# Optimization experiments

Measured on AMD Instinct MI355X. Metric: run time of the kernel, lower is better.

Reference implementation:

```python
import jax, jax.numpy as jnp
import numpy as np

D_MODEL = 1024
NUM_HEADS = 16
D_K = D_MODEL // NUM_HEADS
NEG = -10000.0


def setup_inputs() -> dict:
    key = jax.random.key(0)
    ks = jax.random.split(key, 8)
    B, S = 2, 2048
    query = jax.random.normal(ks[0], (B, S, D_MODEL), dtype=jnp.float32)
    key_t = jax.random.normal(ks[1], (B, S, D_MODEL), dtype=jnp.float32)
    value = jax.random.normal(ks[2], (B, S, D_MODEL), dtype=jnp.float32)
    mask = jax.random.randint(ks[3], (B, S), 0, 2, dtype=jnp.int32)
    scale = 1.0 / np.sqrt(D_MODEL)
    Wq = jax.random.normal(ks[4], (D_MODEL, D_MODEL), dtype=jnp.float32) * scale
    Wk = jax.random.normal(ks[5], (D_MODEL, D_MODEL), dtype=jnp.float32) * scale
    Wv = jax.random.normal(ks[6], (D_MODEL, D_MODEL), dtype=jnp.float32) * scale
    Wo = jax.random.normal(ks[7], (D_MODEL, D_MODEL), dtype=jnp.float32) * scale
    return {"query": query, "key": key_t, "value": value, "mask": mask,
            "Wq": Wq, "Wk": Wk, "Wv": Wv, "Wo": Wo}


def reference(query, key, value, mask, Wq, Wk, Wv, Wo):
    B, Sq, _ = query.shape
    Sk = key.shape[1]
    # Linear projections (torch Linear: x @ W.T), split heads -> [B,H,S,d_k]
    def proj(x, W, S):
        return (x @ W.T).reshape(B, S, NUM_HEADS, D_K).transpose(0, 2, 1, 3)
    Q = proj(query, Wq, Sq)
    K = proj(key, Wk, Sk)
    V = proj(value, Wv, Sk)
    # scores [B,H,Sq,Sk]
    scores = jnp.einsum("bhqd,bhkd->bhqk", Q, K) / jnp.sqrt(jnp.float32(D_K))
    # padding mask [B,Sk] -> [B,1,1,Sk]
    pad = mask[:, None, None, :]
    scores = jnp.where(pad == 0, NEG, scores)
    # causal mask (mask_future=True)
    causal = jnp.tril(jnp.ones((Sq, Sk), dtype=bool))
    scores = jnp.where(causal, scores, NEG)
    probs = jax.nn.softmax(scores, axis=-1)  # dropout p=0.0 -> identity
    out = jnp.einsum("bhqk,bhkd->bhqd", probs, V)
    out = out.transpose(0, 2, 1, 3).reshape(B, Sq, D_MODEL)
    return out @ Wo.T
```

## Files before the change

kernel.cpp:

```cpp
#include <hip/hip_runtime.h>
#include <hip/hip_bf16.h>
#include <math.h>

typedef __attribute__((ext_vector_type(8))) short s16x8;
typedef __attribute__((ext_vector_type(4))) float f32x4;

#define MFMA16(a,b,c) __builtin_amdgcn_mfma_f32_16x16x32_bf16((a),(b),(c),0,0,0)

#define GLD16(gp, lp) __builtin_amdgcn_global_load_lds( \
  (const __attribute__((address_space(1))) unsigned int*)(gp), \
  (__attribute__((address_space(3))) unsigned int*)(lp), 16, 0, 0)

static __device__ __forceinline__ unsigned short f2bu(float f) {
  __hip_bfloat16 h = __float2bfloat16(f);
  unsigned short u; __builtin_memcpy(&u, &h, 2); return u;
}
static __device__ __forceinline__ float b2f(unsigned short u) {
  unsigned int x = ((unsigned int)u) << 16; float f; __builtin_memcpy(&f, &x, 4); return f;
}
static __device__ __forceinline__ unsigned int cvtpk(float lo, float hi) {
  unsigned int r;
  asm("v_cvt_pk_bf16_f32 %0, %1, %2" : "=v"(r) : "v"(lo), "v"(hi));
  return r;
}

__global__ __launch_bounds__(256) void cast_all(const float* __restrict__ q, const float* __restrict__ k,
                                                const float* __restrict__ v,
                                                const float* __restrict__ Wq, const float* __restrict__ Wk,
                                                const float* __restrict__ Wv, const float* __restrict__ Wo,
                                                const int* __restrict__ mask,
                                                unsigned short* __restrict__ qc, unsigned short* __restrict__ kc,
                                                unsigned short* __restrict__ vc,
                                                unsigned short* __restrict__ wq, unsigned short* __restrict__ wk,
                                                unsigned short* __restrict__ wv, unsigned short* __restrict__ wo,
                                                int* __restrict__ fu, unsigned int* __restrict__ pm) {
  const float SCALE2 = 0.125f * 1.4426950408889634f;
  const int y = blockIdx.y;
  if (y == 7) {
    if (blockIdx.x >= 2) return;
    const int S = 2048;
    int b = blockIdx.x;
    __shared__ int red[256];
    int best = S;
    for (int kk = threadIdx.x; kk < 1024; kk += 256) {
      int m0 = mask[b * S + 2 * kk], m1 = mask[b * S + 2 * kk + 1];
      pm[b * 1024 + kk] = (m0 ? 0xFFFFu : 0u) | (m1 ? 0xFFFF0000u : 0u);
      if (m1) best = min(best, 2 * kk + 1);
      if (m0) best = min(best, 2 * kk);
    }
    red[threadIdx.x] = best;
    __syncthreads();
    for (int s = 128; s > 0; s >>= 1) {
      if (threadIdx.x < s) red[threadIdx.x] = min(red[threadIdx.x], red[threadIdx.x + s]);
      __syncthreads();
    }
    if (threadIdx.x == 0) fu[b] = red[0];
    return;
  }
  const float* in; unsigned short* out; int n4; float scl = 1.0f;
  switch (y) {
    case 0: in = q;  out = qc; n4 = 1048576; break;
    case 1: in = k;  out = kc; n4 = 1048576; break;
    case 2: in = v;  out = vc; n4 = 1048576; break;
    case 3: in = Wq; out = wq; n4 = 262144; scl = SCALE2; break;
    case 4: in = Wk; out = wk; n4 = 262144; break;
    case 5: in = Wv; out = wv; n4 = 262144; break;
    default: in = Wo; out = wo; n4 = 262144; break;
  }
  int i = blockIdx.x * 256 + threadIdx.x;
  if (i < n4) {
    float4 val = *(const float4*)(in + (size_t)i * 4);
    uint2 pk;
    pk.x = cvtpk(val.x * scl, val.y * scl);
    pk.y = cvtpk(val.z * scl, val.w * scl);
    *(uint2*)(out + (size_t)i * 4) = pk;
  }
}

static __device__ __forceinline__ void gemm_core(const unsigned short* __restrict__ Aw,
                                                 const unsigned short* __restrict__ Bw,
                                                 int m0, int n0,
                                                 f32x4 (&acc)[4][4],
                                                 unsigned short (*As)[64], unsigned short (*Bs)[64]) {
  const int K = 1024;
  const int tid = threadIdx.x;
  const int lane = tid & 63, wave = tid >> 6;
  const int wm = wave >> 1, wn = wave & 1;
  const int row16 = lane & 15, kgrp = lane >> 4;
  const int srow = lane >> 3, sslot = (lane & 7) ^ srow;
  const int sw = row16 & 7;

  for (int k0 = 0; k0 < K; k0 += 64) {
#pragma unroll
    for (int i = 0; i < 4; i++) {
      int rr = (wave * 4 + i) * 8 + srow;
      GLD16(Aw + (size_t)(m0 + rr) * K + k0 + sslot * 8, (char*)As + (wave * 4 + i) * 1024);
      GLD16(Bw + (size_t)(n0 + rr) * K + k0 + sslot * 8, (char*)Bs + (wave * 4 + i) * 1024);
    }
    __syncthreads();

#pragma unroll
    for (int kk = 0; kk < 2; kk++) {
      s16x8 af[4], bfr[4];
#pragma unroll
      for (int mi = 0; mi < 4; mi++) {
        int rr = wm * 64 + mi * 16 + row16;
        af[mi] = *(const s16x8*)((char*)&As[rr][0] + ((kk * 4 + kgrp) ^ sw) * 16);
      }
#pragma unroll
      for (int ni = 0; ni < 4; ni++) {
        int rr = wn * 64 + ni * 16 + row16;
        bfr[ni] = *(const s16x8*)((char*)&Bs[rr][0] + ((kk * 4 + kgrp) ^ sw) * 16);
      }
#pragma unroll
      for (int mi = 0; mi < 4; mi++)
#pragma unroll
        for (int ni = 0; ni < 4; ni++)
          acc[mi][ni] = MFMA16(af[mi], bfr[ni], acc[mi][ni]);
    }
    __syncthreads();
  }
}

__global__ __launch_bounds__(256) void qkv_gemm(const unsigned short* __restrict__ qc,
                                                const unsigned short* __restrict__ kc,
                                                const unsigned short* __restrict__ vc,
                                                const unsigned short* __restrict__ Wqb,
                                                const unsigned short* __restrict__ Wkb,
                                                const unsigned short* __restrict__ Wvb,
                                                unsigned short* __restrict__ Qb,
                                                unsigned short* __restrict__ Kb,
                                                unsigned short* __restrict__ Vt) {
  __shared__ unsigned short As[128][64];
  __shared__ unsigned short Bs[128][64];
  const int xcd = blockIdx.x & 7, u = blockIdx.x >> 3;
  const int g = xcd * 12 + (u >> 3);
  const int z = g >> 5, mstrip = g & 31;
  const int m0 = mstrip * 128, n0 = (u & 7) * 128;

  const unsigned short* A = (z == 0) ? qc : (z == 1) ? kc : vc;
  const unsigned short* Bw = (z == 0) ? Wqb : (z == 1) ? Wkb : Wvb;

  f32x4 acc[4][4] = {};
  gemm_core(A, Bw, m0, n0, acc, As, Bs);

  const int lane = threadIdx.x & 63, wave = threadIdx.x >> 6;
  const int wm = wave >> 1, wn = wave & 1;
  const int row16 = lane & 15, kgrp = lane >> 4;

  if (z < 2) {
    unsigned short* C = z ? Kb : Qb;
#pragma unroll
    for (int mi = 0; mi < 4; mi++)
#pragma unroll
      for (int ni = 0; ni < 4; ni++)
#pragma unroll
        for (int r = 0; r < 4; r++) {
          int row = m0 + wm * 64 + mi * 16 + kgrp * 4 + r;
          int col = n0 + wn * 64 + ni * 16 + row16;
          C[(size_t)row * 1024 + col] = f2bu(acc[mi][ni][r]);
        }
  } else {
#pragma unroll
    for (int mi = 0; mi < 4; mi++)
#pragma unroll
      for (int ni = 0; ni < 4; ni++) {
        int mb = m0 + wm * 64 + mi * 16 + kgrp * 4;
        int col = n0 + wn * 64 + ni * 16 + row16;
        int bb = mb >> 11, s = mb & 2047;
        uint2 pk;
        pk.x = cvtpk(acc[mi][ni][0], acc[mi][ni][1]);
        pk.y = cvtpk(acc[mi][ni][2], acc[mi][ni][3]);
        *(uint2*)&Vt[(((size_t)(bb * 1024 + col)) << 11) + s] = pk;
      }
  }
}

__global__ __launch_bounds__(256) void gemm_wo(const unsigned short* __restrict__ A,
                                               const unsigned short* __restrict__ Bw,
                                               float* __restrict__ C) {
  __shared__ unsigned short As[128][64];
  __shared__ unsigned short Bs[128][64];
  const int xcd = blockIdx.x & 7, u = blockIdx.x >> 3;
  const int g = xcd * 4 + (u >> 3);
  const int m0 = g * 128, n0 = (u & 7) * 128;

  f32x4 acc[4][4] = {};
  gemm_core(A, Bw, m0, n0, acc, As, Bs);

  const int lane = threadIdx.x & 63, wave = threadIdx.x >> 6;
  const int wm = wave >> 1, wn = wave & 1;
  const int row16 = lane & 15, kgrp = lane >> 4;
#pragma unroll
  for (int mi = 0; mi < 4; mi++)
#pragma unroll
    for (int ni = 0; ni < 4; ni++)
#pragma unroll
      for (int r = 0; r < 4; r++) {
        int row = m0 + wm * 64 + mi * 16 + kgrp * 4 + r;
        int col = n0 + wn * 64 + ni * 16 + row16;
        C[(size_t)row * 1024 + col] = acc[mi][ni][r];
      }
}

__global__ __launch_bounds__(256) void reduce_vt(const unsigned short* __restrict__ Vt,
                                                 float* __restrict__ vsum) {
  __shared__ float red[256];
  const unsigned short* p = Vt + ((size_t)blockIdx.x << 11) + threadIdx.x * 8;
  uint4 u = *(const uint4*)p;
  float s = b2f((unsigned short)(u.x & 0xffff));
  s += b2f((unsigned short)(u.x >> 16));
  s += b2f((unsigned short)(u.y & 0xffff));
  s += b2f((unsigned short)(u.y >> 16));
  s += b2f((unsigned short)(u.z & 0xffff));
  s += b2f((unsigned short)(u.z >> 16));
  s += b2f((unsigned short)(u.w & 0xffff));
  s += b2f((unsigned short)(u.w >> 16));
  red[threadIdx.x] = s;
  __syncthreads();
  for (int st = 128; st > 0; st >>= 1) {
    if (threadIdx.x < st) red[threadIdx.x] += red[threadIdx.x + st];
    __syncthreads();
  }
  if (threadIdx.x == 0) vsum[blockIdx.x] = red[0];
}

__global__ __launch_bounds__(256) void flash_attn8(const unsigned short* __restrict__ Q,
                                                   const unsigned short* __restrict__ Kp,
                                                   const unsigned short* __restrict__ Vt,
                                                   const unsigned int* __restrict__ pm,
                                                   const int* __restrict__ fu,
                                                   const float* __restrict__ vsum,
                                                   unsigned short* __restrict__ O) {
  const int S = 2048, DM = 1024;
  const int bid = blockIdx.x;
  const int qt = 31 - (bid >> 5);
  const int bh = bid & 31;
  const int b = bh >> 4, h = bh & 15;
  const int tid = threadIdx.x, lane = tid & 63, wave = tid >> 6;
  const int row16 = lane & 15, kgrp = lane >> 4;

  __shared__ unsigned short Ks[2][64][64];
  __shared__ unsigned short Vs[2][64][64];
  __shared__ unsigned short Ps[4][16][64];

  const size_t base = ((size_t)b * S) * DM + h * 64;
  const size_t vtb = ((size_t)(b * 1024 + h * 64)) * S;
  const unsigned int* pmb = pm + b * 1024;

  const int srow = lane >> 3;
  const int sslot = (lane & 7) ^ srow;
  const int sw = row16 & 7;

  const int q0 = qt * 64 + wave * 16;
  const int qg = q0 + row16;
  const int nt = qt + 1;

  s16x8 qf0 = *(const s16x8*)&Q[base + (size_t)qg * DM + kgrp * 8];
  s16x8 qf1 = *(const s16x8*)&Q[base + (size_t)qg * DM + 32 + kgrp * 8];

  const short ONE = 0x3F80;
  const s16x8 ones8 = {ONE, ONE, ONE, ONE, ONE, ONE, ONE, ONE};

  f32x4 oacc[4] = {};
  f32x4 lacc = {};
  float m_run = -1e30f;

  auto stage = [&](int t, int bf) {
    const int kb = t * 64;
#pragma unroll
    for (int c2 = 0; c2 < 2; c2++) {
      const int r = wave * 16 + c2 * 8 + srow;
      GLD16(Kp + base + (size_t)(kb + r) * DM + sslot * 8,
            (char*)&Ks[bf][0][0] + (wave * 2 + c2) * 1024);
      GLD16(Vt + vtb + (size_t)r * S + kb + sslot * 8,
            (char*)&Vs[bf][0][0] + (wave * 2 + c2) * 1024);
    }
  };

  stage(0, 0);
  asm volatile("s_waitcnt vmcnt(0)" ::: "memory");
  __syncthreads();

  int cur = 0;
  for (int t = 0; t < nt; ++t) {
    if (t + 1 < nt) stage(t + 1, cur ^ 1);
    const int kb = t * 64;

    uint2 pmv[4];
#pragma unroll
    for (int nf = 0; nf < 4; nf++)
      pmv[nf] = *(const uint2*)&pmb[(kb + nf * 16 + kgrp * 4) >> 1];

    f32x4 sc[4];
    __builtin_amdgcn_s_setprio(1);
#pragma unroll
    for (int nf = 0; nf < 4; nf++) {
      const int rr = nf * 16 + row16;
      s16x8 k0 = *(const s16x8*)&Ks[cur][rr][(kgrp ^ sw) * 8];
      s16x8 k1 = *(const s16x8*)&Ks[cur][rr][((4 + kgrp) ^ sw) * 8];
      f32x4 a = {};
      a = MFMA16(k0, qf0, a);
      a = MFMA16(k1, qf1, a);
      sc[nf] = a;
    }
    __builtin_amdgcn_s_setprio(0);

    if (t == nt - 1) {
#pragma unroll
      for (int nf = 0; nf < 4; nf++) {
        const int kbase = kb + nf * 16 + kgrp * 4;
#pragma unroll
        for (int r = 0; r < 4; r++)
          if (kbase + r > qg) sc[nf][r] = -30000.0f;
      }
    }

    float a0 = fmaxf(fmaxf(sc[0][0], sc[0][1]), sc[0][2]);
    float a1 = fmaxf(fmaxf(sc[0][3], sc[1][0]), sc[1][1]);
    float a2 = fmaxf(fmaxf(sc[1][2], sc[1][3]), sc[2][0]);
    float a3 = fmaxf(fmaxf(sc[2][1], sc[2][2]), sc[2][3]);
    float a4 = fmaxf(fmaxf(sc[3][0], sc[3][1]), sc[3][2]);
    float b0 = fmaxf(fmaxf(a0, a1), a2);
    float b1 = fmaxf(fmaxf(a3, a4), sc[3][3]);
    float tmax = fmaxf(b0, b1);

    if (__any(tmax > m_run)) {
      float wmax = fmaxf(tmax, __shfl_xor(tmax, 16));
      wmax = fmaxf(wmax, __shfl_xor(wmax, 32));
      float alpha = __builtin_exp2f(m_run - wmax);
      m_run = wmax;
      lacc[0] *= alpha; lacc[1] *= alpha; lacc[2] *= alpha; lacc[3] *= alpha;
#pragma unroll
      for (int nf2 = 0; nf2 < 4; nf2++)
#pragma unroll
        for (int r = 0; r < 4; r++) oacc[nf2][r] *= alpha;
    }

#pragma unroll
    for (int nf = 0; nf < 4; nf++)
#pragma unroll
      for (int r = 0; r < 4; r++)
        sc[nf][r] = __builtin_exp2f(sc[nf][r] - m_run);

#pragma unroll
    for (int nf = 0; nf < 4; nf++) {
      uint2 pk;
      pk.x = cvtpk(sc[nf][0], sc[nf][1]) & pmv[nf].x;
      pk.y = cvtpk(sc[nf][2], sc[nf][3]) & pmv[nf].y;
      const int slot = (nf * 2 + (kgrp >> 1)) ^ sw;
      *(uint2*)((char*)&Ps[wave][row16][0] + slot * 16 + (kgrp & 1) * 8) = pk;
    }
    s16x8 pf0 = *(const s16x8*)((char*)&Ps[wave][row16][0] + (kgrp ^ sw) * 16);
    s16x8 pf1 = *(const s16x8*)((char*)&Ps[wave][row16][0] + ((4 + kgrp) ^ sw) * 16);

    __builtin_amdgcn_s_setprio(1);
    lacc = MFMA16(ones8, pf0, lacc);
    lacc = MFMA16(ones8, pf1, lacc);
#pragma unroll
    for (int nf2 = 0; nf2 < 4; nf2++) {
      const int rr = nf2 * 16 + row16;
      s16x8 v0 = *(const s16x8*)&Vs[cur][rr][(kgrp ^ sw) * 8];
      s16x8 v1 = *(const s16x8*)&Vs[cur][rr][((4 + kgrp) ^ sw) * 8];
      oacc[nf2] = MFMA16(v0, pf0, oacc[nf2]);
      oacc[nf2] = MFMA16(v1, pf1, oacc[nf2]);
    }
    __builtin_amdgcn_s_setprio(0);

    asm volatile("s_waitcnt vmcnt(0)" ::: "memory");
    __syncthreads();
    cur ^= 1;
  }

  const int fub = fu[b];
  const float* vs = vsum + b * DM + h * 64;
  const float rl = 1.0f / lacc[0];
#pragma unroll
  for (int nf2 = 0; nf2 < 4; nf2++) {
    const int d0 = nf2 * 16 + kgrp * 4;
    float v0 = oacc[nf2][0] * rl, v1 = oacc[nf2][1] * rl;
    float v2 = oacc[nf2][2] * rl, v3 = oacc[nf2][3] * rl;
    if (qg < fub) {
      float4 vv = *(const float4*)&vs[d0];
      v0 = vv.x * (1.0f / 2048.0f);
      v1 = vv.y * (1.0f / 2048.0f);
      v2 = vv.z * (1.0f / 2048.0f);
      v3 = vv.w * (1.0f / 2048.0f);
    }
    uint2 pk;
    pk.x = cvtpk(v0, v1);
    pk.y = cvtpk(v2, v3);
    *(uint2*)&O[base + (size_t)qg * DM + d0] = pk;
  }
}

extern "C" void kernel_launch(void* const* d_in, const int* in_sizes, int n_in,
                              void* d_out, int out_size, void* d_ws, size_t ws_size,
                              hipStream_t stream) {
  const float* q    = (const float*)d_in[0];
  const float* k    = (const float*)d_in[1];
  const float* v    = (const float*)d_in[2];
  const int*   mask = (const int*)d_in[3];
  const float* Wq   = (const float*)d_in[4];
  const float* Wk   = (const float*)d_in[5];
  const float* Wv   = (const float*)d_in[6];
  const float* Wo   = (const float*)d_in[7];
  float* out = (float*)d_out;
  char* ws = (char*)d_ws;

  unsigned short* Wqb  = (unsigned short*)(ws + (size_t)0);
  unsigned short* Wkb  = (unsigned short*)(ws + ((size_t)2 << 20));
  unsigned short* Wvb  = (unsigned short*)(ws + ((size_t)4 << 20));
  unsigned short* Wob  = (unsigned short*)(ws + ((size_t)6 << 20));
  unsigned short* vc   = (unsigned short*)(ws + ((size_t)8 << 20));
  unsigned short* attn = (unsigned short*)(ws + ((size_t)8 << 20));
  unsigned short* Qb   = (unsigned short*)(ws + ((size_t)16 << 20));
  unsigned short* Kb   = (unsigned short*)(ws + ((size_t)24 << 20));
  unsigned short* Vt   = (unsigned short*)(ws + ((size_t)32 << 20));
  float* vsum          = (float*)(ws + ((size_t)40 << 20));
  int*   fub           = (int*)(ws + ((size_t)40 << 20) + (64 << 10));
  unsigned int* pm32   = (unsigned int*)(ws + ((size_t)40 << 20) + (68 << 10));
  unsigned short* qc   = (unsigned short*)d_out;
  unsigned short* kc   = (unsigned short*)d_out + 4194304;

  cast_all<<<dim3(4096, 8), 256, 0, stream>>>(q, k, v, Wq, Wk, Wv, Wo, mask,
                                              qc, kc, vc, Wqb, Wkb, Wvb, Wob, fub, pm32);

  qkv_gemm<<<768, 256, 0, stream>>>(qc, kc, vc, Wqb, Wkb, Wvb, Qb, Kb, Vt);

  reduce_vt<<<2048, 256, 0, stream>>>(Vt, vsum);

  flash_attn8<<<1024, 256, 0, stream>>>(Qb, Kb, Vt, pm32, fub, vsum, attn);

  gemm_wo<<<256, 256, 0, stream>>>(attn, Wob, out);
}
```

Baseline: 140.9 us.

## Process two 16-row query fragments per wave to double K/V tile reuse

Each wave now handles 32 query rows (two 16-row MFMA fragments) instead of 16, so each block covers a 128-row query tile and the grid halves to 512 blocks. Every K and V tile staged into LDS, and every K/V fragment read from LDS, now feeds twice as many MFMAs, which cuts global and LDS traffic per unit of compute. The causal mask now applies to the last two key tiles. The cost is higher register pressure from doubled accumulators and query fragments, fewer blocks to spread across CUs, and coarser causal load imbalance.

```diff
diff --git a/kernel.cpp b/kernel.cpp
--- a/kernel.cpp
+++ b/kernel.cpp
@@ -225,7 +225,7 @@
   if (threadIdx.x == 0) vsum[blockIdx.x] = red[0];
 }
 
-__global__ __launch_bounds__(256) void flash_attn8(const unsigned short* __restrict__ Q,
+__global__ __launch_bounds__(256) void flash_attn9(const unsigned short* __restrict__ Q,
                                                    const unsigned short* __restrict__ Kp,
                                                    const unsigned short* __restrict__ Vt,
                                                    const unsigned int* __restrict__ pm,
@@ -234,7 +234,7 @@
                                                    unsigned short* __restrict__ O) {
   const int S = 2048, DM = 1024;
   const int bid = blockIdx.x;
-  const int qt = 31 - (bid >> 5);
+  const int qtile = 15 - (bid >> 5);
   const int bh = bid & 31;
   const int b = bh >> 4, h = bh & 15;
   const int tid = threadIdx.x, lane = tid & 63, wave = tid >> 6;
@@ -242,7 +242,7 @@
 
   __shared__ unsigned short Ks[2][64][64];
   __shared__ unsigned short Vs[2][64][64];
-  __shared__ unsigned short Ps[4][16][64];
+  __shared__ unsigned short Ps[4][32][64];
 
   const size_t base = ((size_t)b * S) * DM + h * 64;
   const size_t vtb = ((size_t)(b * 1024 + h * 64)) * S;
@@ -252,19 +252,23 @@
   const int sslot = (lane & 7) ^ srow;
   const int sw = row16 & 7;
 
-  const int q0 = qt * 64 + wave * 16;
-  const int qg = q0 + row16;
-  const int nt = qt + 1;
-
-  s16x8 qf0 = *(const s16x8*)&Q[base + (size_t)qg * DM + kgrp * 8];
-  s16x8 qf1 = *(const s16x8*)&Q[base + (size_t)qg * DM + 32 + kgrp * 8];
+  const int q0w = qtile * 128 + wave * 32;
+  int qgF[2]; qgF[0] = q0w + row16; qgF[1] = q0w + 16 + row16;
+  const int nt = qtile * 2 + 2;
+
+  s16x8 qf[2][2];
+#pragma unroll
+  for (int f = 0; f < 2; f++) {
+    qf[f][0] = *(const s16x8*)&Q[base + (size_t)qgF[f] * DM + kgrp * 8];
+    qf[f][1] = *(const s16x8*)&Q[base + (size_t)qgF[f] * DM + 32 + kgrp * 8];
+  }
 
   const short ONE = 0x3F80;
   const s16x8 ones8 = {ONE, ONE, ONE, ONE, ONE, ONE, ONE, ONE};
 
-  f32x4 oacc[4] = {};
-  f32x4 lacc = {};
-  float m_run = -1e30f;
+  f32x4 oacc[2][4] = {};
+  f32x4 lacc[2] = {};
+  float m_run[2] = {-1e30f, -1e30f};
 
   auto stage = [&](int t, int bf) {
     const int kb = t * 64;
@@ -292,78 +296,92 @@
     for (int nf = 0; nf < 4; nf++)
       pmv[nf] = *(const uint2*)&pmb[(kb + nf * 16 + kgrp * 4) >> 1];
 
-    f32x4 sc[4];
+    f32x4 sc[2][4];
     __builtin_amdgcn_s_setprio(1);
 #pragma unroll
     for (int nf = 0; nf < 4; nf++) {
       const int rr = nf * 16 + row16;
       s16x8 k0 = *(const s16x8*)&Ks[cur][rr][(kgrp ^ sw) * 8];
       s16x8 k1 = *(const s16x8*)&Ks[cur][rr][((4 + kgrp) ^ sw) * 8];
-      f32x4 a = {};
-      a = MFMA16(k0, qf0, a);
-      a = MFMA16(k1, qf1, a);
-      sc[nf] = a;
+      f32x4 aA = {}, aB = {};
+      aA = MFMA16(k0, qf[0][0], aA);
+      aA = MFMA16(k1, qf[0][1], aA);
+      aB = MFMA16(k0, qf[1][0], aB);
+      aB = MFMA16(k1, qf[1][1], aB);
+      sc[0][nf] = aA; sc[1][nf] = aB;
     }
     __builtin_amdgcn_s_setprio(0);
 
-    if (t == nt - 1) {
+    if (t >= nt - 2) {
+#pragma unroll
+      for (int f = 0; f < 2; f++)
+#pragma unroll
+        for (int nf = 0; nf < 4; nf++) {
+          const int kbase = kb + nf * 16 + kgrp * 4;
+#pragma unroll
+          for (int r = 0; r < 4; r++)
+            if (kbase + r > qgF[f]) sc[f][nf][r] = -30000.0f;
+        }
+    }
+
+    s16x8 pf[2][2];
+#pragma unroll
+    for (int f = 0; f < 2; f++) {
+      float a0 = fmaxf(fmaxf(sc[f][0][0], sc[f][0][1]), sc[f][0][2]);
+      float a1 = fmaxf(fmaxf(sc[f][0][3], sc[f][1][0]), sc[f][1][1]);
+      float a2 = fmaxf(fmaxf(sc[f][1][2], sc[f][1][3]), sc[f][2][0]);
+      float a3 = fmaxf(fmaxf(sc[f][2][1], sc[f][2][2]), sc[f][2][3]);
+      float a4 = fmaxf(fmaxf(sc[f][3][0], sc[f][3][1]), sc[f][3][2]);
+      float b0 = fmaxf(fmaxf(a0, a1), a2);
+      float b1 = fmaxf(fmaxf(a3, a4), sc[f][3][3]);
+      float tmax = fmaxf(b0, b1);
+
+      if (__any(tmax > m_run[f])) {
+        float wmax = fmaxf(tmax, __shfl_xor(tmax, 16));
+        wmax = fmaxf(wmax, __shfl_xor(wmax, 32));
+        float alpha = __builtin_exp2f(m_run[f] - wmax);
+        m_run[f] = wmax;
+        lacc[f][0] *= alpha; lacc[f][1] *= alpha; lacc[f][2] *= alpha; lacc[f][3] *= alpha;
+#pragma unroll
+        for (int nf2 = 0; nf2 < 4; nf2++)
+#pragma unroll
+          for (int r = 0; r < 4; r++) oacc[f][nf2][r] *= alpha;
+      }
+
+#pragma unroll
+      for (int nf = 0; nf < 4; nf++)
+#pragma unroll
+        for (int r = 0; r < 4; r++)
+          sc[f][nf][r] = __builtin_exp2f(sc[f][nf][r] - m_run[f]);
+
+      char* prow = (char*)&Ps[wave][f * 16 + row16][0];
 #pragma unroll
       for (int nf = 0; nf < 4; nf++) {
-        const int kbase = kb + nf * 16 + kgrp * 4;
-#pragma unroll
-        for (int r = 0; r < 4; r++)
-          if (kbase + r > qg) sc[nf][r] = -30000.0f;
-      }
-    }
-
-    float a0 = fmaxf(fmaxf(sc[0][0], sc[0][1]), sc[0][2]);
-    float a1 = fmaxf(fmaxf(sc[0][3], sc[1][0]), sc[1][1]);
-    float a2 = fmaxf(fmaxf(sc[1][2], sc[1][3]), sc[2][0]);
-    float a3 = fmaxf(fmaxf(sc[2][1], sc[2][2]), sc[2][3]);
-    float a4 = fmaxf(fmaxf(sc[3][0], sc[3][1]), sc[3][2]);
-    float b0 = fmaxf(fmaxf(a0, a1), a2);
-    float b1 = fmaxf(fmaxf(a3, a4), sc[3][3]);
-    float tmax = fmaxf(b0, b1);
-
-    if (__any(tmax > m_run)) {
-      float wmax = fmaxf(tmax, __shfl_xor(tmax, 16));
-      wmax = fmaxf(wmax, __shfl_xor(wmax, 32));
-      float alpha = __builtin_exp2f(m_run - wmax);
-      m_run = wmax;
-      lacc[0] *= alpha; lacc[1] *= alpha; lacc[2] *= alpha; lacc[3] *= alpha;
-#pragma unroll
-      for (int nf2 = 0; nf2 < 4; nf2++)
-#pragma unroll
-        for (int r = 0; r < 4; r++) oacc[nf2][r] *= alpha;
-    }
-
-#pragma unroll
-    for (int nf = 0; nf < 4; nf++)
-#pragma unroll
-      for (int r = 0; r < 4; r++)
-        sc[nf][r] = __builtin_exp2f(sc[nf][r] - m_run);
-
-#pragma unroll
-    for (int nf = 0; nf < 4; nf++) {
-      uint2 pk;
-      pk.x = cvtpk(sc[nf][0], sc[nf][1]) & pmv[nf].x;
-      pk.y = cvtpk(sc[nf][2], sc[nf][3]) & pmv[nf].y;
-      const int slot = (nf * 2 + (kgrp >> 1)) ^ sw;
-      *(uint2*)((char*)&Ps[wave][row16][0] + slot * 16 + (kgrp & 1) * 8) = pk;
-    }
-    s16x8 pf0 = *(const s16x8*)((char*)&Ps[wave][row16][0] + (kgrp ^ sw) * 16);
-    s16x8 pf1 = *(const s16x8*)((char*)&Ps[wave][row16][0] + ((4 + kgrp) ^ sw) * 16);
+        uint2 pk;
+        pk.x = cvtpk(sc[f][nf][0], sc[f][nf][1]) & pmv[nf].x;
+        pk.y = cvtpk(sc[f][nf][2], sc[f][nf][3]) & pmv[nf].y;
+        const int slot = (nf * 2 + (kgrp >> 1)) ^ sw;
+        *(uint2*)(prow + slot * 16 + (kgrp & 1) * 8) = pk;
+      }
+      pf[f][0] = *(const s16x8*)(prow + (kgrp ^ sw) * 16);
+      pf[f][1] = *(const s16x8*)(prow + ((4 + kgrp) ^ sw) * 16);
+    }
 
     __builtin_amdgcn_s_setprio(1);
-    lacc = MFMA16(ones8, pf0, lacc);
-    lacc = MFMA16(ones8, pf1, lacc);
+#pragma unroll
+    for (int f = 0; f < 2; f++) {
+      lacc[f] = MFMA16(ones8, pf[f][0], lacc[f]);
+      lacc[f] = MFMA16(ones8, pf[f][1], lacc[f]);
+    }
 #pragma unroll
     for (int nf2 = 0; nf2 < 4; nf2++) {
       const int rr = nf2 * 16 + row16;
       s16x8 v0 = *(const s16x8*)&Vs[cur][rr][(kgrp ^ sw) * 8];
       s16x8 v1 = *(const s16x8*)&Vs[cur][rr][((4 + kgrp) ^ sw) * 8];
-      oacc[nf2] = MFMA16(v0, pf0, oacc[nf2]);
-      oacc[nf2] = MFMA16(v1, pf1, oacc[nf2]);
+      oacc[0][nf2] = MFMA16(v0, pf[0][0], oacc[0][nf2]);
+      oacc[0][nf2] = MFMA16(v1, pf[0][1], oacc[0][nf2]);
+      oacc[1][nf2] = MFMA16(v0, pf[1][0], oacc[1][nf2]);
+      oacc[1][nf2] = MFMA16(v1, pf[1][1], oacc[1][nf2]);
     }
     __builtin_amdgcn_s_setprio(0);
 
@@ -374,23 +392,27 @@
 
   const int fub = fu[b];
   const float* vs = vsum + b * DM + h * 64;
-  const float rl = 1.0f / lacc[0];
-#pragma unroll
-  for (int nf2 = 0; nf2 < 4; nf2++) {
-    const int d0 = nf2 * 16 + kgrp * 4;
-    float v0 = oacc[nf2][0] * rl, v1 = oacc[nf2][1] * rl;
-    float v2 = oacc[nf2][2] * rl, v3 = oacc[nf2][3] * rl;
-    if (qg < fub) {
-      float4 vv = *(const float4*)&vs[d0];
-      v0 = vv.x * (1.0f / 2048.0f);
-      v1 = vv.y * (1.0f / 2048.0f);
-      v2 = vv.z * (1.0f / 2048.0f);
-      v3 = vv.w * (1.0f / 2048.0f);
-    }
-    uint2 pk;
-    pk.x = cvtpk(v0, v1);
-    pk.y = cvtpk(v2, v3);
-    *(uint2*)&O[base + (size_t)qg * DM + d0] = pk;
+#pragma unroll
+  for (int f = 0; f < 2; f++) {
+    const float rl = 1.0f / lacc[f][0];
+    const int qg = qgF[f];
+#pragma unroll
+    for (int nf2 = 0; nf2 < 4; nf2++) {
+      const int d0 = nf2 * 16 + kgrp * 4;
+      float v0 = oacc[f][nf2][0] * rl, v1 = oacc[f][nf2][1] * rl;
+      float v2 = oacc[f][nf2][2] * rl, v3 = oacc[f][nf2][3] * rl;
+      if (qg < fub) {
+        float4 vv = *(const float4*)&vs[d0];
+        v0 = vv.x * (1.0f / 2048.0f);
+        v1 = vv.y * (1.0f / 2048.0f);
+        v2 = vv.z * (1.0f / 2048.0f);
+        v3 = vv.w * (1.0f / 2048.0f);
+      }
+      uint2 pk;
+      pk.x = cvtpk(v0, v1);
+      pk.y = cvtpk(v2, v3);
+      *(uint2*)&O[base + (size_t)qg * DM + d0] = pk;
+    }
   }
 }
 
@@ -430,7 +452,7 @@
 
   reduce_vt<<<2048, 256, 0, stream>>>(Vt, vsum);
 
-  flash_attn8<<<1024, 256, 0, stream>>>(Qb, Kb, Vt, pm32, fub, vsum, attn);
+  flash_attn9<<<512, 256, 0, stream>>>(Qb, Kb, Vt, pm32, fub, vsum, attn);
 
   gemm_wo<<<256, 256, 0, stream>>>(attn, Wob, out);
 }
```

Measured after the change: 162.0 us. +15.0%, slower.

## Split long causal query tiles across two blocks with a combine kernel

Applied to the files above, without the earlier changes.

The upper half of query tiles (qt 16-31), which have the longest causal KV loops, is now processed by two blocks, each covering half of the KV tiles. The blocks write unnormalized partial outputs plus running max and sum to scratch. A new combine kernel merges each pair with log-sum-exp weighting and applies the uniform-row fallback. This evens out per-block work across the causal triangle and adds blocks to cut tail imbalance, at the cost of an extra launch and fp32 partial traffic that reuses the output buffer as scratch.

```diff
diff --git a/kernel.cpp b/kernel.cpp
--- a/kernel.cpp
+++ b/kernel.cpp
@@ -225,21 +225,35 @@
   if (threadIdx.x == 0) vsum[blockIdx.x] = red[0];
 }
 
-__global__ __launch_bounds__(256) void flash_attn8(const unsigned short* __restrict__ Q,
-                                                   const unsigned short* __restrict__ Kp,
-                                                   const unsigned short* __restrict__ Vt,
-                                                   const unsigned int* __restrict__ pm,
-                                                   const int* __restrict__ fu,
-                                                   const float* __restrict__ vsum,
-                                                   unsigned short* __restrict__ O) {
+__global__ __launch_bounds__(256) void flash_attn10(const unsigned short* __restrict__ Q,
+                                                    const unsigned short* __restrict__ Kp,
+                                                    const unsigned short* __restrict__ Vt,
+                                                    const unsigned int* __restrict__ pm,
+                                                    const int* __restrict__ fu,
+                                                    const float* __restrict__ vsum,
+                                                    unsigned short* __restrict__ O,
+                                                    float* __restrict__ pO,
+                                                    float* __restrict__ pML) {
   const int S = 2048, DM = 1024;
   const int bid = blockIdx.x;
-  const int qt = 31 - (bid >> 5);
-  const int bh = bid & 31;
+  const int j = bid >> 5, bh = bid & 31;
   const int b = bh >> 4, h = bh & 15;
   const int tid = threadIdx.x, lane = tid & 63, wave = tid >> 6;
   const int row16 = lane & 15, kgrp = lane >> 4;
 
+  int qt, t0, t1, half = 0;
+  if (j < 32) {
+    qt = 31 - (j >> 1);
+    half = j & 1;
+    const int n = qt + 1, nA = (n + 1) >> 1;
+    t0 = half ? nA : 0;
+    t1 = half ? n : nA;
+  } else {
+    qt = 47 - j;
+    t0 = 0;
+    t1 = qt + 1;
+  }
+
   __shared__ unsigned short Ks[2][64][64];
   __shared__ unsigned short Vs[2][64][64];
   __shared__ unsigned short Ps[4][16][64];
@@ -252,9 +266,8 @@
   const int sslot = (lane & 7) ^ srow;
   const int sw = row16 & 7;
 
-  const int q0 = qt * 64 + wave * 16;
-  const int qg = q0 + row16;
-  const int nt = qt + 1;
+  const int qloc = wave * 16 + row16;
+  const int qg = qt * 64 + qloc;
 
   s16x8 qf0 = *(const s16x8*)&Q[base + (size_t)qg * DM + kgrp * 8];
   s16x8 qf1 = *(const s16x8*)&Q[base + (size_t)qg * DM + 32 + kgrp * 8];
@@ -278,13 +291,13 @@
     }
   };
 
-  stage(0, 0);
+  stage(t0, 0);
   asm volatile("s_waitcnt vmcnt(0)" ::: "memory");
   __syncthreads();
 
   int cur = 0;
-  for (int t = 0; t < nt; ++t) {
-    if (t + 1 < nt) stage(t + 1, cur ^ 1);
+  for (int t = t0; t < t1; ++t) {
+    if (t + 1 < t1) stage(t + 1, cur ^ 1);
     const int kb = t * 64;
 
     uint2 pmv[4];
@@ -306,7 +319,7 @@
     }
     __builtin_amdgcn_s_setprio(0);
 
-    if (t == nt - 1) {
+    if (t == qt) {
 #pragma unroll
       for (int nf = 0; nf < 4; nf++) {
         const int kbase = kb + nf * 16 + kgrp * 4;
@@ -372,16 +385,85 @@
     cur ^= 1;
   }
 
+  if (j < 32) {
+    const int p = (((bh << 4) + (qt - 16)) << 1) + half;
+    float* po = pO + ((size_t)p << 12) + (size_t)qloc * 64;
+#pragma unroll
+    for (int nf2 = 0; nf2 < 4; nf2++) {
+      const int d0 = nf2 * 16 + kgrp * 4;
+      float4 vv;
+      vv.x = oacc[nf2][0]; vv.y = oacc[nf2][1];
+      vv.z = oacc[nf2][2]; vv.w = oacc[nf2][3];
+      *(float4*)&po[d0] = vv;
+    }
+    if (kgrp == 0) {
+      float2 mlv; mlv.x = m_run; mlv.y = lacc[0];
+      *(float2*)&pML[(p << 7) + qloc * 2] = mlv;
+    }
+  } else {
+    const int fub = fu[b];
+    const float* vs = vsum + b * DM + h * 64;
+    const float rl = 1.0f / lacc[0];
+#pragma unroll
+    for (int nf2 = 0; nf2 < 4; nf2++) {
+      const int d0 = nf2 * 16 + kgrp * 4;
+      float v0 = oacc[nf2][0] * rl, v1 = oacc[nf2][1] * rl;
+      float v2 = oacc[nf2][2] * rl, v3 = oacc[nf2][3] * rl;
+      if (qg < fub) {
+        float4 vv = *(const float4*)&vs[d0];
+        v0 = vv.x * (1.0f / 2048.0f);
+        v1 = vv.y * (1.0f / 2048.0f);
+        v2 = vv.z * (1.0f / 2048.0f);
+        v3 = vv.w * (1.0f / 2048.0f);
+      }
+      uint2 pk;
+      pk.x = cvtpk(v0, v1);
+      pk.y = cvtpk(v2, v3);
+      *(uint2*)&O[base + (size_t)qg * DM + d0] = pk;
+    }
+  }
+}
+
+__global__ __launch_bounds__(256) void combine_k(const float* __restrict__ pO,
+                                                 const float* __restrict__ pML,
+                                                 const int* __restrict__ fu,
+                                                 const float* __restrict__ vsum,
+                                                 unsigned short* __restrict__ O) {
+  const int S = 2048, DM = 1024;
+  const int g = blockIdx.x;
+  const int bh = g >> 4, qti = g & 15;
+  const int b = bh >> 4, h = bh & 15;
+  const int qt = 16 + qti;
+  const int p0 = ((bh << 4) + qti) << 1;
+  const int tid = threadIdx.x;
+  const int qloc = tid >> 2, d0 = (tid & 3) << 4;
+  const int qg = qt * 64 + qloc;
+
+  float2 ml0 = *(const float2*)&pML[(p0 << 7) + qloc * 2];
+  float2 ml1 = *(const float2*)&pML[((p0 + 1) << 7) + qloc * 2];
+  float m = fmaxf(ml0.x, ml1.x);
+  float w0 = __builtin_exp2f(ml0.x - m);
+  float w1 = __builtin_exp2f(ml1.x - m);
+  float l = w0 * ml0.y + w1 * ml1.y;
+  float rl = 1.0f / l;
+
   const int fub = fu[b];
+  const bool uni = qg < fub;
   const float* vs = vsum + b * DM + h * 64;
-  const float rl = 1.0f / lacc[0];
-#pragma unroll
-  for (int nf2 = 0; nf2 < 4; nf2++) {
-    const int d0 = nf2 * 16 + kgrp * 4;
-    float v0 = oacc[nf2][0] * rl, v1 = oacc[nf2][1] * rl;
-    float v2 = oacc[nf2][2] * rl, v3 = oacc[nf2][3] * rl;
-    if (qg < fub) {
-      float4 vv = *(const float4*)&vs[d0];
+  const float* o0 = pO + ((size_t)p0 << 12) + (size_t)qloc * 64 + d0;
+  const float* o1 = o0 + 4096;
+  unsigned short* dst = O + ((size_t)(b * S + qg)) * DM + h * 64 + d0;
+
+#pragma unroll
+  for (int i = 0; i < 4; i++) {
+    float4 a = *(const float4*)&o0[i * 4];
+    float4 c = *(const float4*)&o1[i * 4];
+    float v0 = (w0 * a.x + w1 * c.x) * rl;
+    float v1 = (w0 * a.y + w1 * c.y) * rl;
+    float v2 = (w0 * a.z + w1 * c.z) * rl;
+    float v3 = (w0 * a.w + w1 * c.w) * rl;
+    if (uni) {
+      float4 vv = *(const float4*)&vs[d0 + i * 4];
       v0 = vv.x * (1.0f / 2048.0f);
       v1 = vv.y * (1.0f / 2048.0f);
       v2 = vv.z * (1.0f / 2048.0f);
@@ -390,7 +472,7 @@
     uint2 pk;
     pk.x = cvtpk(v0, v1);
     pk.y = cvtpk(v2, v3);
-    *(uint2*)&O[base + (size_t)qg * DM + d0] = pk;
+    *(uint2*)&dst[i * 4] = pk;
   }
 }
 
@@ -420,8 +502,10 @@
   float* vsum          = (float*)(ws + ((size_t)40 << 20));
   int*   fub           = (int*)(ws + ((size_t)40 << 20) + (64 << 10));
   unsigned int* pm32   = (unsigned int*)(ws + ((size_t)40 << 20) + (68 << 10));
+  float* pML           = (float*)(ws + ((size_t)41 << 20));
   unsigned short* qc   = (unsigned short*)d_out;
   unsigned short* kc   = (unsigned short*)d_out + 4194304;
+  float* pO            = (float*)d_out;
 
   cast_all<<<dim3(4096, 8), 256, 0, stream>>>(q, k, v, Wq, Wk, Wv, Wo, mask,
                                               qc, kc, vc, Wqb, Wkb, Wvb, Wob, fub, pm32);
@@ -430,7 +514,9 @@
 
   reduce_vt<<<2048, 256, 0, stream>>>(Vt, vsum);
 
-  flash_attn8<<<1024, 256, 0, stream>>>(Qb, Kb, Vt, pm32, fub, vsum, attn);
+  flash_attn10<<<1536, 256, 0, stream>>>(Qb, Kb, Vt, pm32, fub, vsum, attn, pO, pML);
+
+  combine_k<<<512, 256, 0, stream>>>(pO, pML, fub, vsum, attn);
 
   gemm_wo<<<256, 256, 0, stream>>>(attn, Wob, out);
 }
```

Result: slower. 152.2 us (+8.0%).
